# Kernel tuning notes

Hardware: AMD Instinct MI355X
Metric: run time of the kernel (lower is better)

Reference implementation:

```python
import jax, jax.numpy as jnp
import numpy as np

BEV_H = 512
BEV_W = 512


def setup_inputs() -> dict:
    key = jax.random.key(0)
    k1, k2, k3, k4 = jax.random.split(key, 4)
    P, C, B = 200000, 64, 4
    pillar_feats = jax.random.normal(k1, (P, C), dtype=jnp.float32)
    b_idx = jax.random.randint(k2, (P,), 0, B, dtype=jnp.int32)
    r_idx = jax.random.randint(k3, (P,), 0, BEV_H, dtype=jnp.int32)
    c_idx = jax.random.randint(k4, (P,), 0, BEV_W, dtype=jnp.int32)
    coords = jnp.stack([b_idx, r_idx, c_idx], axis=1)  # (P, 3) int32
    return {"pillar_feats": pillar_feats, "coords": coords, "batch_size": B}


def reference(pillar_feats, coords, batch_size):
    # pillar_feats: (P, C) float; coords: (P, 3) int (batch, row, col)
    H, W = BEV_H, BEV_W
    P, C = pillar_feats.shape
    b = coords[:, 0].astype(jnp.int32)
    r = jnp.clip(coords[:, 1].astype(jnp.int32), 0, H - 1)
    c = jnp.clip(coords[:, 2].astype(jnp.int32), 0, W - 1)
    flat_key = b * (H * W) + r * W + c  # (P,)
    # index that maps to it (equivalent to the module's dedup + unique scatter).
    last = jnp.full((batch_size * H * W,), -1, dtype=jnp.int32)
    last = last.at[flat_key].max(jnp.arange(P, dtype=jnp.int32))  # (B*H*W,)
    valid = last >= 0
    gathered = pillar_feats[jnp.clip(last, 0)]  # (B*H*W, C)
    bev_flat = jnp.where(valid[:, None], gathered, jnp.zeros((), pillar_feats.dtype))
    bev = bev_flat.reshape(batch_size, H, W, C).transpose(0, 3, 1, 2)  # (B, C, H, W)
    return bev
```

## Files before the change

kernel.cpp:

```cpp
#include <hip/hip_runtime.h>

#define BEV_H 512
#define BEV_W 512
#define CCH   64
#define HW    (BEV_H * BEV_W)
#define CHW   (CCH * HW)

#define CELLS   128
#define THREADS 256

__global__ void bev_fill_neg1(int* __restrict__ out_i, int B) {
    int t = blockIdx.x * blockDim.x + threadIdx.x;
    const int per_b4 = HW / 4;
    if (t >= B * per_b4) return;
    int b  = t / per_b4;
    int i4 = t - b * per_b4;
    int4* p = reinterpret_cast<int4*>(out_i + (size_t)b * CHW);
    p[i4] = make_int4(-1, -1, -1, -1);
}

__global__ void bev_scatter_max(const int* __restrict__ coords,
                                int* __restrict__ out_i, int P) {
    int p = blockIdx.x * blockDim.x + threadIdx.x;
    if (p >= P) return;
    int b = coords[p * 3 + 0];
    int r = coords[p * 3 + 1];
    int c = coords[p * 3 + 2];
    r = min(max(r, 0), BEV_H - 1);
    c = min(max(c, 0), BEV_W - 1);
    size_t key = (size_t)b * CHW + (size_t)r * BEV_W + c;
    atomicMax(&out_i[key], p);
}

__global__ __launch_bounds__(THREADS, 4)
void bev_gather(const float* __restrict__ feats, float* __restrict__ out) {
    __shared__ float tile[CELLS][CCH + 1];
    __shared__ int   shwin[CELLS];

    const int t    = threadIdx.x;
    const int blk  = blockIdx.x;
    const int cell0 = blk * CELLS;
    const int c0   = cell0 & (BEV_W - 1);
    const int br   = cell0 / BEV_W;
    const int b    = br >> 9;
    const int r    = br & (BEV_H - 1);

    const int* winplane = reinterpret_cast<const int*>(out)
                        + (size_t)b * CHW + (size_t)r * BEV_W + c0;
    if (t < CELLS) shwin[t] = winplane[t];
    __syncthreads();

    const int w     = t >> 6;
    const int l     = t & 63;
    const int chunk = l & 15;
    const int sub   = l >> 4;
#pragma unroll
    for (int it = 0; it < CELLS / 16; ++it) {
        int cell = it * 16 + w * 4 + sub;
        int win  = shwin[cell];
        float4 v = make_float4(0.f, 0.f, 0.f, 0.f);
        if (win >= 0)
            v = *reinterpret_cast<const float4*>(
                    feats + (size_t)win * CCH + chunk * 4);
        *reinterpret_cast<float4*>(&tile[cell][chunk * 4]) = v;
    }
    __syncthreads();

    const int ch = t >> 2;
    const int q  = t & 3;
    float* chbase = out + (size_t)b * CHW + (size_t)ch * HW
                  + (size_t)r * BEV_W + c0;
#pragma unroll
    for (int i = 0; i < 8; ++i) {
        int cell = i * 16 + q * 4;
        float4 v = make_float4(tile[cell + 0][ch], tile[cell + 1][ch],
                               tile[cell + 2][ch], tile[cell + 3][ch]);
        *reinterpret_cast<float4*>(chbase + cell) = v;
    }
}

extern "C" void kernel_launch(void* const* d_in, const int* in_sizes, int n_in,
                              void* d_out, int out_size, void* d_ws, size_t ws_size,
                              hipStream_t stream) {
    const float* feats  = (const float*)d_in[0];
    const int*   coords = (const int*)d_in[1];

    const int P = in_sizes[0] / CCH;
    const int B = out_size / CHW;
    const int ncell = B * HW;

    float* out  = (float*)d_out;
    int*   outi = (int*)d_out;

    {
        int n = ncell / 4;
        int blocks = (n + 255) / 256;
        bev_fill_neg1<<<blocks, 256, 0, stream>>>(outi, B);
    }
    {
        int blocks = (P + 255) / 256;
        bev_scatter_max<<<blocks, 256, 0, stream>>>(coords, outi, P);
    }
    {
        int blocks = ncell / CELLS;
        bev_gather<<<blocks, THREADS, 0, stream>>>(feats, out);
    }
}
```

Before: 359.3 us.

## Gather per channel plane reading winner indices directly, drop shared-memory transpose

Replaces the shared-memory transpose gather with a kernel where each block writes a region of one channel plane. It reads winner indices from channel 0 of the output and does scalar strided gathers of one feature channel. Channels 1..63 go first, then a second launch overwrites channel 0, which also holds the indices. Stores are nontemporal. The cost is that every channel plane rereads the index plane and the feature gathers become uncoalesced scalar loads.

```diff
diff --git a/kernel.cpp b/kernel.cpp
--- a/kernel.cpp
+++ b/kernel.cpp
@@ -6,8 +6,12 @@
 #define HW    (BEV_H * BEV_W)
 #define CHW   (CCH * HW)
 
-#define CELLS   128
 #define THREADS 256
+#define REGIONS 8
+#define RFLOATS (HW / REGIONS)
+#define ITERS   (RFLOATS / (THREADS * 4))
+
+typedef float f32x4 __attribute__((ext_vector_type(4)));
 
 __global__ void bev_fill_neg1(int* __restrict__ out_i, int B) {
     int t = blockIdx.x * blockDim.x + threadIdx.x;
@@ -32,50 +36,32 @@
     atomicMax(&out_i[key], p);
 }
 
-__global__ __launch_bounds__(THREADS, 4)
-void bev_gather(const float* __restrict__ feats, float* __restrict__ out) {
-    __shared__ float tile[CELLS][CCH + 1];
-    __shared__ int   shwin[CELLS];
+__global__ __launch_bounds__(THREADS)
+void bev_gather_planes(const float* __restrict__ feats,
+                       float* __restrict__ out, int ch_base) {
+    const int region = blockIdx.x;
+    const int ch     = ch_base + blockIdx.y;
+    const int b      = blockIdx.z;
 
-    const int t    = threadIdx.x;
-    const int blk  = blockIdx.x;
-    const int cell0 = blk * CELLS;
-    const int c0   = cell0 & (BEV_W - 1);
-    const int br   = cell0 / BEV_W;
-    const int b    = br >> 9;
-    const int r    = br & (BEV_H - 1);
+    const int t = threadIdx.x;
+    const int base = region * RFLOATS;
 
-    const int* winplane = reinterpret_cast<const int*>(out)
-                        + (size_t)b * CHW + (size_t)r * BEV_W + c0;
-    if (t < CELLS) shwin[t] = winplane[t];
-    __syncthreads();
+    const int*  winplane = reinterpret_cast<const int*>(out) + (size_t)b * CHW;
+    const float* f_ch    = feats + ch;
+    float* outplane      = out + (size_t)b * CHW + (size_t)ch * HW;
 
-    const int w     = t >> 6;
-    const int l     = t & 63;
-    const int chunk = l & 15;
-    const int sub   = l >> 4;
-#pragma unroll
-    for (int it = 0; it < CELLS / 16; ++it) {
-        int cell = it * 16 + w * 4 + sub;
-        int win  = shwin[cell];
-        float4 v = make_float4(0.f, 0.f, 0.f, 0.f);
-        if (win >= 0)
-            v = *reinterpret_cast<const float4*>(
-                    feats + (size_t)win * CCH + chunk * 4);
-        *reinterpret_cast<float4*>(&tile[cell][chunk * 4]) = v;
-    }
-    __syncthreads();
+#pragma unroll 4
+    for (int it = 0; it < ITERS; ++it) {
+        int idx = base + it * (THREADS * 4) + t * 4;
+        const int4 w4 = *reinterpret_cast<const int4*>(winplane + idx);
 
-    const int ch = t >> 2;
-    const int q  = t & 3;
-    float* chbase = out + (size_t)b * CHW + (size_t)ch * HW
-                  + (size_t)r * BEV_W + c0;
-#pragma unroll
-    for (int i = 0; i < 8; ++i) {
-        int cell = i * 16 + q * 4;
-        float4 v = make_float4(tile[cell + 0][ch], tile[cell + 1][ch],
-                               tile[cell + 2][ch], tile[cell + 3][ch]);
-        *reinterpret_cast<float4*>(chbase + cell) = v;
+        f32x4 v = (f32x4)(0.f);
+        if (w4.x >= 0) v.x = f_ch[(size_t)w4.x * CCH];
+        if (w4.y >= 0) v.y = f_ch[(size_t)w4.y * CCH];
+        if (w4.z >= 0) v.z = f_ch[(size_t)w4.z * CCH];
+        if (w4.w >= 0) v.w = f_ch[(size_t)w4.w * CCH];
+
+        __builtin_nontemporal_store(v, reinterpret_cast<f32x4*>(outplane + idx));
     }
 }
 
@@ -102,7 +88,11 @@
         bev_scatter_max<<<blocks, 256, 0, stream>>>(coords, outi, P);
     }
     {
-        int blocks = ncell / CELLS;
-        bev_gather<<<blocks, THREADS, 0, stream>>>(feats, out);
+        dim3 grid(REGIONS, CCH - 1, B);
+        bev_gather_planes<<<grid, THREADS, 0, stream>>>(feats, out, 1);
+    }
+    {
+        dim3 grid(REGIONS, 1, B);
+        bev_gather_planes<<<grid, THREADS, 0, stream>>>(feats, out, 0);
     }
 }
```

New measurement: 414.0 us. +15.2%, slower.
